# Kernel optimization log

Measured on AMD Instinct MI355X. Metric: run time of the kernel, lower is better.

Reference implementation:

```python
import jax, jax.numpy as jnp
import numpy as np

N_EMBED = 512  # codebook size per Quantize
EPS = 1e-8


def _quantize(x, embed):
    # x: (L, d) flattened tokens; embed: (d, K) codebook
    # squared euclidean distance via expansion (as in torch source)
    dist = (x * x).sum(1, keepdims=True) - 2.0 * (x @ embed) + (embed * embed).sum(0, keepdims=True)
    ind = jnp.argmin(dist, axis=1)                      # (L,)
    q = jnp.take(embed.T, ind, axis=0)                  # (L, d) embedding lookup
    diff = jnp.mean((jax.lax.stop_gradient(q) - x) ** 2)
    q_st = x + jax.lax.stop_gradient(q - x)             # straight-through
    return q_st, diff, ind


def _ot_score(x, embed):
    # x: (L, d); embed: (d, K). OT score = sum_k (1 - cos_sim) * softmax(x@embed / K)
    xn = x / (jnp.linalg.norm(x, axis=1, keepdims=True) + EPS)
    en = embed / (jnp.linalg.norm(embed, axis=0, keepdims=True) + EPS)
    cos_dissim = jax.lax.stop_gradient(1.0 - xn @ en)   # torch version uses .data (no grad)
    cnd = jax.nn.softmax((x @ embed) * (1.0 / embed.shape[1]), axis=1)
    return (cos_dissim * cnd).sum(1)                    # (L,)


def setup_inputs() -> dict:
    key = jax.random.key(0)
    k1, k2, k3, k4 = jax.random.split(key, 4)
    n_levels, B, L, d = 5, 128, 196, 64
    input_list = jax.random.normal(k1, (n_levels, B, L, d), dtype=jnp.float32)
    cb_top = jax.random.normal(k2, (15, d, N_EMBED), dtype=jnp.float32)        # quantize_list_5
    cb_lvl = jax.random.normal(k3, (4, 15, 2 * d, N_EMBED), dtype=jnp.float32)  # quantize_list_1..4
    label = jax.random.randint(k4, (B,), 0, 15, dtype=jnp.int32)
    return {"input_list": input_list, "cb_top": cb_top, "cb_lvl": cb_lvl, "label": label}


def reference(input_list, cb_top, cb_lvl, label):
    # Hierarchical switch-VQ encode (eval mode): top level quantized with per-class
    # codebook, then each lower level concatenated with top quantized code and
    # quantized with its own per-class codebook; last level also computes OT score.
    vq = jax.vmap(_quantize)
    emb_top = cb_top[label]                              # (B, 64, 512) per-sample codebook
    q4, d4, _ = vq(input_list[4], emb_top)               # (B, L, 64)
    diff = d4.sum()
    quants, ids = [], []
    ot_score = None
    for j in (3, 2, 1, 0):                               # quantize_list_4, _3, _2, _1
        x = jnp.concatenate([input_list[j], q4], axis=-1)  # (B, L, 128)
        emb = cb_lvl[j][label]                           # (B, 128, 512)
        q, d, i = vq(x, emb)
        diff = diff + d.sum()
        quants.append(q)
        ids.append(i)
        if j == 0:                                       # OT=True level
            ot_score = jax.vmap(_ot_score)(x, emb)       # (B, L)
    quant_list = jnp.stack(quants)                       # (4, B, L, 128)
    id_list = jnp.stack(ids)                             # (4, B, L)
    return quant_list, diff, id_list, ot_score
```

## Files before the change

kernel.cpp:

```cpp
#include <hip/hip_runtime.h>
#include <hip/hip_bf16.h>
#include <math.h>

#define B 128
#define L 196
#define K 512
#define NCLS 15
#define NT 32
#define NTILES 7

#define DIFF_OFF 12845056
#define ID_OFF   12845057
#define OT_OFF   12945409

#define WS_N2   0
#define WS_INVE 38400
#define WS_CBT  46080
#define CBT_LVL 491520
#define WS_EBT_BYTES ((size_t)(46080 + 4469760) * 4)
#define EBT_LVL_BYTES 983040

#define BAND 2.5f
#define CCAP 512

typedef __attribute__((ext_vector_type(8))) short s16x8;
typedef __attribute__((ext_vector_type(4))) float f32x4;
typedef __attribute__((ext_vector_type(4))) unsigned short u16x4;

__device__ inline unsigned short f2bf(float f) {
    __hip_bfloat16 h = __float2bfloat16(f);
    return *reinterpret_cast<unsigned short*>(&h);
}

__global__ __launch_bounds__(256) void precompute(
    const float* __restrict__ cb_top, const float* __restrict__ cb_lvl,
    float* __restrict__ ws)
{
    __shared__ float Ld[128][65];
    __shared__ float ps[64][4];
    const int m = blockIdx.x >> 3;
    const int c0 = (blockIdx.x & 7) * 64;
    const bool top = m < NCLS;
    const int D = top ? 64 : 128;
    const float* src = top ? cb_top + (size_t)m * 64 * K
                           : cb_lvl + (size_t)(m - NCLS) * 128 * K;
    float* cbT = ws + WS_CBT + (top ? (size_t)m * K * 64
                                    : (size_t)CBT_LVL + (size_t)(m - NCLS) * K * 128);
    unsigned short* ebt = (unsigned short*)((char*)ws + WS_EBT_BYTES +
        (top ? (size_t)m * K * 64 * 2
             : (size_t)EBT_LVL_BYTES + (size_t)(m - NCLS) * K * 128 * 2));
    const int tid = threadIdx.x;

    for (int e = tid; e < D * 64; e += 256) {
        int d = e >> 6, cc = e & 63;
        Ld[d][cc] = src[(size_t)d * K + c0 + cc];
    }
    __syncthreads();

    const int col = tid >> 2, q = tid & 3;
    const int seg = D >> 2;
    float ss = 0.f;
    for (int i = 0; i < seg; ++i) {
        int d = q * seg + i;
        float v = Ld[d][col];
        ss = fmaf(v, v, ss);
        cbT[(size_t)(c0 + col) * D + d] = v;
        ebt[(size_t)(c0 + col) * D + d] = f2bf(v);
    }
    ps[col][q] = ss;
    __syncthreads();
    if (tid < 64) {
        float n2 = (ps[tid][0] + ps[tid][1]) + (ps[tid][2] + ps[tid][3]);
        ws[WS_N2 + (size_t)m * K + c0 + tid] = n2;
        if (m >= NCLS && m < 2 * NCLS)
            ws[WS_INVE + (size_t)(m - NCLS) * K + c0 + tid] = 1.f / (sqrtf(n2) + 1e-8f);
    }
}

__global__ __launch_bounds__(256, 6) void vq_all(
    const float* __restrict__ input, const int* __restrict__ label,
    float* __restrict__ ws, float* __restrict__ out)
{
    __shared__ char uA[8192];
    __shared__ unsigned short xL_s[NT * 136];
    __shared__ float clv[CCAP];
    __shared__ unsigned int clist[CCAP];
    __shared__ float wmin_s[4][NT];
    __shared__ float rowMinG[NT];
    __shared__ unsigned long long best_s[NT];
    __shared__ float xn4_s[NT], xnL_s[NT], xnq_s[NT];
    __shared__ float otZ_s[NT], otW_s[NT];
    __shared__ float dacc_s;
    __shared__ int ccnt;

    unsigned short* x4_s = (unsigned short*)uA;
    float* q4f = (float*)uA;

    const int tid = threadIdx.x;
    const int t0 = blockIdx.x * NT;
    const int b = blockIdx.y;
    const int j = blockIdx.z;
    const bool OT = (j == 0);
    const bool addTop = (j == 3);
    const int c = label[b];

    const float* xin4 = input + ((size_t)(4 * B + b) * L) * 64;
    const float* xinj = input + ((size_t)(j * B + b) * L) * 64;
    const float* n2T = ws + WS_N2 + (size_t)c * K;
    const float* n2L = ws + WS_N2 + (size_t)(NCLS + j * NCLS + c) * K;
    const float* ive = ws + WS_INVE + (size_t)c * K;
    const float* cbT_T = ws + WS_CBT + (size_t)c * (K * 64);
    const float* cbT_L = ws + WS_CBT + CBT_LVL + (size_t)(j * NCLS + c) * (K * 128);
    const unsigned short* ebT =
        (const unsigned short*)((const char*)ws + WS_EBT_BYTES) + (size_t)c * (K * 64);
    const unsigned short* ebL =
        (const unsigned short*)((const char*)ws + WS_EBT_BYTES + EBT_LVL_BYTES) +
        (size_t)(j * NCLS + c) * (K * 128);

    const int wid = tid >> 6, lane = tid & 63, l15 = lane & 15, l4 = lane >> 4;

    if (tid < NT) {
        xn4_s[tid] = 0.f; xnL_s[tid] = 0.f; best_s[tid] = ~0ULL;
        otZ_s[tid] = 0.f; otW_s[tid] = 0.f;
    }
    if (tid == 0) { ccnt = 0; dacc_s = 0.f; }
    __syncthreads();

    for (int idx = tid; idx < NT * 16; idx += 256) {
        int row = idx >> 4, k4 = (idx & 15) << 2;
        int l = t0 + row;
        float4 v = make_float4(0.f, 0.f, 0.f, 0.f);
        if (l < L) {
            v = *(const float4*)(xin4 + (size_t)l * 64 + k4);
            atomicAdd(&xn4_s[row], v.x * v.x + v.y * v.y + v.z * v.z + v.w * v.w);
        }
        u16x4 h; h[0] = f2bf(v.x); h[1] = f2bf(v.y); h[2] = f2bf(v.z); h[3] = f2bf(v.w);
        *(u16x4*)&x4_s[row * 72 + k4] = h;
    }
    __syncthreads();

    float runMin[2][4];
    #pragma unroll
    for (int mi = 0; mi < 2; ++mi)
        #pragma unroll
        for (int r = 0; r < 4; ++r) runMin[mi][r] = 3.4e38f;

    for (int cc = 0; cc < 2; ++cc) {
        const int colbase = cc * 256 + wid * 64;
        float n2v[4];
        #pragma unroll
        for (int ni = 0; ni < 4; ++ni) n2v[ni] = n2T[colbase + ni * 16 + l15];
        f32x4 acc[2][4] = {};
        #pragma unroll
        for (int ks = 0; ks < 2; ++ks) {
            s16x8 av[2], bv[4];
            #pragma unroll
            for (int mi = 0; mi < 2; ++mi)
                av[mi] = *(const s16x8*)&x4_s[(mi * 16 + l15) * 72 + ks * 32 + l4 * 8];
            #pragma unroll
            for (int ni = 0; ni < 4; ++ni)
                bv[ni] = *(const s16x8*)&ebT[(size_t)(colbase + ni * 16 + l15) * 64 + ks * 32 + l4 * 8];
            #pragma unroll
            for (int mi = 0; mi < 2; ++mi)
                #pragma unroll
                for (int ni = 0; ni < 4; ++ni)
                    acc[mi][ni] = __builtin_amdgcn_mfma_f32_16x16x32_bf16(
                        av[mi], bv[ni], acc[mi][ni], 0, 0, 0);
        }
        #pragma unroll
        for (int mi = 0; mi < 2; ++mi) {
            #pragma unroll
            for (int r = 0; r < 4; ++r) {
                const int row = mi * 16 + l4 * 4 + r;
                float dv[4];
                #pragma unroll
                for (int ni = 0; ni < 4; ++ni)
                    dv[ni] = n2v[ni] - 2.f * acc[mi][ni][r];
                float mnW = fminf(fminf(dv[0], dv[1]), fminf(dv[2], dv[3]));
                #pragma unroll
                for (int s = 1; s <= 8; s <<= 1)
                    mnW = fminf(mnW, __shfl_xor(mnW, s, 64));
                runMin[mi][r] = fminf(runMin[mi][r], mnW);
                const float thr = runMin[mi][r] + BAND;
                if (t0 + row < L) {
                    #pragma unroll
                    for (int ni = 0; ni < 4; ++ni) {
                        if (dv[ni] <= thr) {
                            int pos = atomicAdd(&ccnt, 1);
                            if (pos < CCAP) {
                                clist[pos] = ((unsigned)row << 16) |
                                             (unsigned)(colbase + ni * 16 + l15);
                                clv[pos] = dv[ni];
                            }
                        }
                    }
                }
            }
        }
    }
    #pragma unroll
    for (int mi = 0; mi < 2; ++mi)
        #pragma unroll
        for (int r = 0; r < 4; ++r)
            if (l15 == 0) wmin_s[wid][mi * 16 + l4 * 4 + r] = runMin[mi][r];
    __syncthreads();
    if (tid < NT)
        rowMinG[tid] = fminf(fminf(wmin_s[0][tid], wmin_s[1][tid]),
                             fminf(wmin_s[2][tid], wmin_s[3][tid]));
    __syncthreads();

    {
        const int ncand = min(ccnt, CCAP);
        const int g = tid >> 4, li = tid & 15;
        for (int e = g; e < ncand; e += 16) {
            unsigned ent = clist[e];
            int row = ent >> 16, col = ent & 0xFFFF;
            if (clv[e] > rowMinG[row] + BAND) continue;
            int l = t0 + row;
            float4 xv = *(const float4*)(xin4 + (size_t)l * 64 + li * 4);
            float4 ev = *(const float4*)(cbT_T + (size_t)col * 64 + li * 4);
            float prod = xv.x * ev.x + xv.y * ev.y + xv.z * ev.z + xv.w * ev.w;
            #pragma unroll
            for (int s = 1; s <= 8; s <<= 1) prod += __shfl_xor(prod, s, 64);
            if (li == 0) {
                float dvE = n2T[col] - 2.f * prod;
                unsigned u = __float_as_uint(dvE);
                u = (u & 0x80000000u) ? ~u : (u | 0x80000000u);
                atomicMin(&best_s[row], ((unsigned long long)u << 32) | (unsigned)col);
            }
        }
    }
    __syncthreads();

    {
        const int g = tid >> 4, li = tid & 15;
        for (int rr = g; rr < NT; rr += 16) {
            int l = t0 + rr;
            unsigned long long key = best_s[rr];
            float4 ev = make_float4(0.f, 0.f, 0.f, 0.f);
            float dvE = 0.f;
            if (l < L) {
                unsigned col = (unsigned)(key & 0xFFFFFFFFull);
                unsigned u = (unsigned)(key >> 32);
                u = (u & 0x80000000u) ? (u & 0x7FFFFFFFu) : ~u;
                dvE = __uint_as_float(u);
                ev = *(const float4*)(cbT_T + (size_t)col * 64 + li * 4);
            }
            *(float4*)&q4f[rr * 64 + li * 4] = ev;
            u16x4 h; h[0] = f2bf(ev.x); h[1] = f2bf(ev.y); h[2] = f2bf(ev.z); h[3] = f2bf(ev.w);
            *(u16x4*)&xL_s[rr * 136 + 64 + li * 4] = h;
            float qs = ev.x * ev.x + ev.y * ev.y + ev.z * ev.z + ev.w * ev.w;
            #pragma unroll
            for (int s = 1; s <= 8; s <<= 1) qs += __shfl_xor(qs, s, 64);
            if (li == 0) {
                xnq_s[rr] = qs;
                if (addTop && l < L)
                    atomicAdd(&dacc_s, (dvE + xn4_s[rr]) * (1.f / (L * 64.f)));
            }
        }
    }
    __syncthreads();

    if (tid < NT) best_s[tid] = ~0ULL;
    if (tid == 0) ccnt = 0;
    for (int idx = tid; idx < NT * 16; idx += 256) {
        int row = idx >> 4, k4 = (idx & 15) << 2;
        int l = t0 + row;
        float4 v = make_float4(0.f, 0.f, 0.f, 0.f);
        if (l < L) {
            v = *(const float4*)(xinj + (size_t)l * 64 + k4);
            atomicAdd(&xnL_s[row], v.x * v.x + v.y * v.y + v.z * v.z + v.w * v.w);
        }
        u16x4 h; h[0] = f2bf(v.x); h[1] = f2bf(v.y); h[2] = f2bf(v.z); h[3] = f2bf(v.w);
        *(u16x4*)&xL_s[row * 136 + k4] = h;
    }
    __syncthreads();

    #pragma unroll
    for (int mi = 0; mi < 2; ++mi)
        #pragma unroll
        for (int r = 0; r < 4; ++r) runMin[mi][r] = 3.4e38f;

    for (int cc = 0; cc < 2; ++cc) {
        const int colbase = cc * 256 + wid * 64;
        float n2v[4], iv[4];
        #pragma unroll
        for (int ni = 0; ni < 4; ++ni) {
            n2v[ni] = n2L[colbase + ni * 16 + l15];
            if (OT) iv[ni] = ive[colbase + ni * 16 + l15];
        }
        f32x4 acc[2][4] = {};
        #pragma unroll
        for (int ks = 0; ks < 4; ++ks) {
            s16x8 av[2], bv[4];
            #pragma unroll
            for (int mi = 0; mi < 2; ++mi)
                av[mi] = *(const s16x8*)&xL_s[(mi * 16 + l15) * 136 + ks * 32 + l4 * 8];
            #pragma unroll
            for (int ni = 0; ni < 4; ++ni)
                bv[ni] = *(const s16x8*)&ebL[(size_t)(colbase + ni * 16 + l15) * 128 + ks * 32 + l4 * 8];
            #pragma unroll
            for (int mi = 0; mi < 2; ++mi)
                #pragma unroll
                for (int ni = 0; ni < 4; ++ni)
                    acc[mi][ni] = __builtin_amdgcn_mfma_f32_16x16x32_bf16(
                        av[mi], bv[ni], acc[mi][ni], 0, 0, 0);
        }
        #pragma unroll
        for (int mi = 0; mi < 2; ++mi) {
            #pragma unroll
            for (int r = 0; r < 4; ++r) {
                const int row = mi * 16 + l4 * 4 + r;
                float dv[4];
                #pragma unroll
                for (int ni = 0; ni < 4; ++ni)
                    dv[ni] = n2v[ni] - 2.f * acc[mi][ni][r];
                float mnW = fminf(fminf(dv[0], dv[1]), fminf(dv[2], dv[3]));
                #pragma unroll
                for (int s = 1; s <= 8; s <<= 1)
                    mnW = fminf(mnW, __shfl_xor(mnW, s, 64));
                runMin[mi][r] = fminf(runMin[mi][r], mnW);
                const float thr = runMin[mi][r] + BAND;
                if (t0 + row < L) {
                    #pragma unroll
                    for (int ni = 0; ni < 4; ++ni) {
                        if (dv[ni] <= thr) {
                            int pos = atomicAdd(&ccnt, 1);
                            if (pos < CCAP) {
                                clist[pos] = ((unsigned)row << 16) |
                                             (unsigned)(colbase + ni * 16 + l15);
                                clv[pos] = dv[ni];
                            }
                        }
                    }
                }
                if (OT) {
                    float xn = xnL_s[row] + xnq_s[row];
                    float ivx = 1.f / (sqrtf(xn) + 1e-8f);
                    float zloc = 0.f, wloc = 0.f;
                    #pragma unroll
                    for (int ni = 0; ni < 4; ++ni) {
                        float s = acc[mi][ni][r];
                        float e = __expf(s * (1.f / 512.f));
                        zloc += e;
                        wloc += (1.f - s * ivx * iv[ni]) * e;
                    }
                    #pragma unroll
                    for (int s = 1; s <= 8; s <<= 1) {
                        zloc += __shfl_xor(zloc, s, 64);
                        wloc += __shfl_xor(wloc, s, 64);
                    }
                    if (l15 == 0) {
                        atomicAdd(&otZ_s[row], zloc);
                        atomicAdd(&otW_s[row], wloc);
                    }
                }
            }
        }
    }
    #pragma unroll
    for (int mi = 0; mi < 2; ++mi)
        #pragma unroll
        for (int r = 0; r < 4; ++r)
            if (l15 == 0) wmin_s[wid][mi * 16 + l4 * 4 + r] = runMin[mi][r];
    __syncthreads();
    if (tid < NT)
        rowMinG[tid] = fminf(fminf(wmin_s[0][tid], wmin_s[1][tid]),
                             fminf(wmin_s[2][tid], wmin_s[3][tid]));
    __syncthreads();

    {
        const int ncand = min(ccnt, CCAP);
        const int g = tid >> 4, li = tid & 15;
        for (int e = g; e < ncand; e += 16) {
            unsigned ent = clist[e];
            int row = ent >> 16, col = ent & 0xFFFF;
            if (clv[e] > rowMinG[row] + BAND) continue;
            int l = t0 + row;
            int k = li * 8;
            float4 xa, xb;
            if (li < 8) {
                xa = *(const float4*)(xinj + (size_t)l * 64 + k);
                xb = *(const float4*)(xinj + (size_t)l * 64 + k + 4);
            } else {
                xa = *(const float4*)&q4f[row * 64 + (k - 64)];
                xb = *(const float4*)&q4f[row * 64 + (k - 60)];
            }
            float4 ea = *(const float4*)(cbT_L + (size_t)col * 128 + k);
            float4 eb = *(const float4*)(cbT_L + (size_t)col * 128 + k + 4);
            float prod = xa.x * ea.x + xa.y * ea.y + xa.z * ea.z + xa.w * ea.w +
                         xb.x * eb.x + xb.y * eb.y + xb.z * eb.z + xb.w * eb.w;
            #pragma unroll
            for (int s = 1; s <= 8; s <<= 1) prod += __shfl_xor(prod, s, 64);
            if (li == 0) {
                float dvE = n2L[col] - 2.f * prod;
                unsigned u = __float_as_uint(dvE);
                u = (u & 0x80000000u) ? ~u : (u | 0x80000000u);
                atomicMin(&best_s[row], ((unsigned long long)u << 32) | (unsigned)col);
            }
        }
    }
    __syncthreads();

    {
        const int slot = 3 - j;
        const int g = tid >> 4, li = tid & 15;
        for (int rr = g; rr < NT; rr += 16) {
            int l = t0 + rr;
            if (l >= L) continue;
            unsigned long long key = best_s[rr];
            unsigned col = (unsigned)(key & 0xFFFFFFFFull);
            unsigned u = (unsigned)(key >> 32);
            u = (u & 0x80000000u) ? (u & 0x7FFFFFFFu) : ~u;
            float dvE = __uint_as_float(u);
            float4 ea = *(const float4*)(cbT_L + (size_t)col * 128 + li * 8);
            float4 eb = *(const float4*)(cbT_L + (size_t)col * 128 + li * 8 + 4);
            float* dst = out + (((size_t)slot * B + b) * L + l) * 128 + li * 8;
            *(float4*)dst = ea;
            *(float4*)(dst + 4) = eb;
            if (li == 0) {
                out[ID_OFF + ((size_t)slot * B + b) * L + l] = (float)col;
                if (OT) out[OT_OFF + (size_t)b * L + l] = otW_s[rr] / otZ_s[rr];
                atomicAdd(&dacc_s, (dvE + xnL_s[rr] + xnq_s[rr]) * (1.f / (L * 128.f)));
            }
        }
    }
    __syncthreads();
    if (tid == 0) atomicAdd(out + DIFF_OFF, dacc_s);
}

extern "C" void kernel_launch(void* const* d_in, const int* in_sizes, int n_in,
                              void* d_out, int out_size, void* d_ws, size_t ws_size,
                              hipStream_t stream) {
    const float* input  = (const float*)d_in[0];
    const float* cb_top = (const float*)d_in[1];
    const float* cb_lvl = (const float*)d_in[2];
    const int*   label  = (const int*)d_in[3];
    float* out = (float*)d_out;
    float* ws  = (float*)d_ws;

    hipMemsetAsync(out + DIFF_OFF, 0, sizeof(float), stream);

    precompute<<<600, 256, 0, stream>>>(cb_top, cb_lvl, ws);
    vq_all<<<dim3(NTILES, B, 4), 256, 0, stream>>>(input, label, ws, out);
}
```

Measured before the change: 346.1 us.

## Group blocks by class label and stage inputs in shared memory for rescoring

A new small kernel sorts batch indices by label. vq_all then remaps block IDs, using an XCD-aware swizzle, so blocks sharing the same codebook run together and the codebook stays hot in L2. The fp32 input rows for level 4 and level j are also staged in shared memory, so candidate rescoring reads LDS instead of global memory, and the rescoring band is narrowed from 2.5 to 1.0 to cut candidate work. The trade-offs are one extra launch, more shared memory with occupancy lowered to 4 blocks per SIMD, and a narrower band that could miss the true argmin under bf16 error.

```diff
diff --git a/kernel.cpp b/kernel.cpp
--- a/kernel.cpp
+++ b/kernel.cpp
@@ -15,12 +15,14 @@
 
 #define WS_N2   0
 #define WS_INVE 38400
-#define WS_CBT  46080
+#define WS_PERM 46080
+#define WS_LAB  46208
+#define WS_CBT  46336
 #define CBT_LVL 491520
-#define WS_EBT_BYTES ((size_t)(46080 + 4469760) * 4)
+#define WS_EBT_BYTES ((size_t)(46336 + 4423680) * 4)
 #define EBT_LVL_BYTES 983040
 
-#define BAND 2.5f
+#define BAND 1.0f
 #define CCAP 512
 
 typedef __attribute__((ext_vector_type(8))) short s16x8;
@@ -30,6 +32,22 @@
 __device__ inline unsigned short f2bf(float f) {
     __hip_bfloat16 h = __float2bfloat16(f);
     return *reinterpret_cast<unsigned short*>(&h);
+}
+
+__global__ void sort_labels(const int* __restrict__ label, int* __restrict__ perm,
+                            int* __restrict__ lab) {
+    __shared__ int ls[B];
+    const int t = threadIdx.x;
+    ls[t] = label[t];
+    lab[t] = ls[t];
+    __syncthreads();
+    const int mine = ls[t];
+    int r = 0;
+    for (int i = 0; i < B; ++i) {
+        int li = ls[i];
+        r += (li < mine) || (li == mine && i < t);
+    }
+    perm[r] = t;
 }
 
 __global__ __launch_bounds__(256) void precompute(
@@ -77,11 +95,13 @@
     }
 }
 
-__global__ __launch_bounds__(256, 6) void vq_all(
-    const float* __restrict__ input, const int* __restrict__ label,
-    float* __restrict__ ws, float* __restrict__ out)
+__global__ __launch_bounds__(256, 4) void vq_all(
+    const float* __restrict__ input, float* __restrict__ ws,
+    float* __restrict__ out)
 {
-    __shared__ char uA[8192];
+    __shared__ float uA[NT][68];
+    __shared__ float xLf[NT][68];
+    __shared__ unsigned short x4_s[NT * 72];
     __shared__ unsigned short xL_s[NT * 136];
     __shared__ float clv[CCAP];
     __shared__ unsigned int clist[CCAP];
@@ -93,31 +113,33 @@
     __shared__ float dacc_s;
     __shared__ int ccnt;
 
-    unsigned short* x4_s = (unsigned short*)uA;
-    float* q4f = (float*)uA;
-
     const int tid = threadIdx.x;
-    const int t0 = blockIdx.x * NT;
-    const int b = blockIdx.y;
-    const int j = blockIdx.z;
+    const int hw = (int)blockIdx.x + 7 * (int)blockIdx.y + 896 * (int)blockIdx.z;
+    const int logical = (hw & 7) * 448 + (hw >> 3);
+    const int j = logical & 3;
+    const int rest = logical >> 2;
+    const int tile = rest % 7;
+    const int ys = rest / 7;
+    const int b = ((const int*)(ws + WS_PERM))[ys];
+    const int cls = ((const int*)(ws + WS_LAB))[b];
+
     const bool OT = (j == 0);
     const bool addTop = (j == 3);
-    const int c = label[b];
+    const int t0 = tile * NT;
+    const int wid = tid >> 6, lane = tid & 63, l15 = lane & 15, l4 = lane >> 4;
 
     const float* xin4 = input + ((size_t)(4 * B + b) * L) * 64;
     const float* xinj = input + ((size_t)(j * B + b) * L) * 64;
-    const float* n2T = ws + WS_N2 + (size_t)c * K;
-    const float* n2L = ws + WS_N2 + (size_t)(NCLS + j * NCLS + c) * K;
-    const float* ive = ws + WS_INVE + (size_t)c * K;
-    const float* cbT_T = ws + WS_CBT + (size_t)c * (K * 64);
-    const float* cbT_L = ws + WS_CBT + CBT_LVL + (size_t)(j * NCLS + c) * (K * 128);
+    const float* n2T = ws + WS_N2 + (size_t)cls * K;
+    const float* n2L = ws + WS_N2 + (size_t)(NCLS + j * NCLS + cls) * K;
+    const float* ive = ws + WS_INVE + (size_t)cls * K;
+    const float* cbT_T = ws + WS_CBT + (size_t)cls * (K * 64);
+    const float* cbT_L = ws + WS_CBT + CBT_LVL + (size_t)(j * NCLS + cls) * (K * 128);
     const unsigned short* ebT =
-        (const unsigned short*)((const char*)ws + WS_EBT_BYTES) + (size_t)c * (K * 64);
+        (const unsigned short*)((const char*)ws + WS_EBT_BYTES) + (size_t)cls * (K * 64);
     const unsigned short* ebL =
         (const unsigned short*)((const char*)ws + WS_EBT_BYTES + EBT_LVL_BYTES) +
-        (size_t)(j * NCLS + c) * (K * 128);
-
-    const int wid = tid >> 6, lane = tid & 63, l15 = lane & 15, l4 = lane >> 4;
+        (size_t)(j * NCLS + cls) * (K * 128);
 
     if (tid < NT) {
         xn4_s[tid] = 0.f; xnL_s[tid] = 0.f; best_s[tid] = ~0ULL;
@@ -134,8 +156,19 @@
             v = *(const float4*)(xin4 + (size_t)l * 64 + k4);
             atomicAdd(&xn4_s[row], v.x * v.x + v.y * v.y + v.z * v.z + v.w * v.w);
         }
+        *(float4*)&uA[row][k4] = v;
         u16x4 h; h[0] = f2bf(v.x); h[1] = f2bf(v.y); h[2] = f2bf(v.z); h[3] = f2bf(v.w);
         *(u16x4*)&x4_s[row * 72 + k4] = h;
+    }
+    for (int idx = tid; idx < NT * 16; idx += 256) {
+        int row = idx >> 4, k4 = (idx & 15) << 2;
+        int l = t0 + row;
+        float4 v = make_float4(0.f, 0.f, 0.f, 0.f);
+        if (l < L) {
+            v = *(const float4*)(xinj + (size_t)l * 64 + k4);
+            atomicAdd(&xnL_s[row], v.x * v.x + v.y * v.y + v.z * v.z + v.w * v.w);
+        }
+        *(float4*)&xLf[row][k4] = v;
     }
     __syncthreads();
 
@@ -216,8 +249,7 @@
             unsigned ent = clist[e];
             int row = ent >> 16, col = ent & 0xFFFF;
             if (clv[e] > rowMinG[row] + BAND) continue;
-            int l = t0 + row;
-            float4 xv = *(const float4*)(xin4 + (size_t)l * 64 + li * 4);
+            float4 xv = *(const float4*)&uA[row][li * 4];
             float4 ev = *(const float4*)(cbT_T + (size_t)col * 64 + li * 4);
             float prod = xv.x * ev.x + xv.y * ev.y + xv.z * ev.z + xv.w * ev.w;
             #pragma unroll
@@ -234,7 +266,9 @@
 
     {
         const int g = tid >> 4, li = tid & 15;
-        for (int rr = g; rr < NT; rr += 16) {
+        #pragma unroll
+        for (int rr0 = 0; rr0 < NT; rr0 += 16) {
+            const int rr = rr0 + g;
             int l = t0 + rr;
             unsigned long long key = best_s[rr];
             float4 ev = make_float4(0.f, 0.f, 0.f, 0.f);
@@ -246,12 +280,13 @@
                 dvE = __uint_as_float(u);
                 ev = *(const float4*)(cbT_T + (size_t)col * 64 + li * 4);
             }
-            *(float4*)&q4f[rr * 64 + li * 4] = ev;
+            float qs = ev.x * ev.x + ev.y * ev.y + ev.z * ev.z + ev.w * ev.w;
+            #pragma unroll
+            for (int s = 1; s <= 8; s <<= 1) qs += __shfl_xor(qs, s, 64);
+            __syncthreads();
+            *(float4*)&uA[rr][li * 4] = ev;
             u16x4 h; h[0] = f2bf(ev.x); h[1] = f2bf(ev.y); h[2] = f2bf(ev.z); h[3] = f2bf(ev.w);
             *(u16x4*)&xL_s[rr * 136 + 64 + li * 4] = h;
-            float qs = ev.x * ev.x + ev.y * ev.y + ev.z * ev.z + ev.w * ev.w;
-            #pragma unroll
-            for (int s = 1; s <= 8; s <<= 1) qs += __shfl_xor(qs, s, 64);
             if (li == 0) {
                 xnq_s[rr] = qs;
                 if (addTop && l < L)
@@ -265,12 +300,7 @@
     if (tid == 0) ccnt = 0;
     for (int idx = tid; idx < NT * 16; idx += 256) {
         int row = idx >> 4, k4 = (idx & 15) << 2;
-        int l = t0 + row;
-        float4 v = make_float4(0.f, 0.f, 0.f, 0.f);
-        if (l < L) {
-            v = *(const float4*)(xinj + (size_t)l * 64 + k4);
-            atomicAdd(&xnL_s[row], v.x * v.x + v.y * v.y + v.z * v.z + v.w * v.w);
-        }
+        float4 v = *(const float4*)&xLf[row][k4];
         u16x4 h; h[0] = f2bf(v.x); h[1] = f2bf(v.y); h[2] = f2bf(v.z); h[3] = f2bf(v.w);
         *(u16x4*)&xL_s[row * 136 + k4] = h;
     }
@@ -376,18 +406,10 @@
             unsigned ent = clist[e];
             int row = ent >> 16, col = ent & 0xFFFF;
             if (clv[e] > rowMinG[row] + BAND) continue;
-            int l = t0 + row;
-            int k = li * 8;
-            float4 xa, xb;
-            if (li < 8) {
-                xa = *(const float4*)(xinj + (size_t)l * 64 + k);
-                xb = *(const float4*)(xinj + (size_t)l * 64 + k + 4);
-            } else {
-                xa = *(const float4*)&q4f[row * 64 + (k - 64)];
-                xb = *(const float4*)&q4f[row * 64 + (k - 60)];
-            }
-            float4 ea = *(const float4*)(cbT_L + (size_t)col * 128 + k);
-            float4 eb = *(const float4*)(cbT_L + (size_t)col * 128 + k + 4);
+            float4 xa = *(const float4*)&xLf[row][li * 4];
+            float4 xb = *(const float4*)&uA[row][li * 4];
+            float4 ea = *(const float4*)(cbT_L + (size_t)col * 128 + li * 4);
+            float4 eb = *(const float4*)(cbT_L + (size_t)col * 128 + 64 + li * 4);
             float prod = xa.x * ea.x + xa.y * ea.y + xa.z * ea.z + xa.w * ea.w +
                          xb.x * eb.x + xb.y * eb.y + xb.z * eb.z + xb.w * eb.w;
             #pragma unroll
@@ -413,11 +435,11 @@
             unsigned u = (unsigned)(key >> 32);
             u = (u & 0x80000000u) ? (u & 0x7FFFFFFFu) : ~u;
             float dvE = __uint_as_float(u);
-            float4 ea = *(const float4*)(cbT_L + (size_t)col * 128 + li * 8);
-            float4 eb = *(const float4*)(cbT_L + (size_t)col * 128 + li * 8 + 4);
-            float* dst = out + (((size_t)slot * B + b) * L + l) * 128 + li * 8;
-            *(float4*)dst = ea;
-            *(float4*)(dst + 4) = eb;
+            float4 ea = *(const float4*)(cbT_L + (size_t)col * 128 + li * 4);
+            float4 eb = *(const float4*)(cbT_L + (size_t)col * 128 + 64 + li * 4);
+            float* dst = out + (((size_t)slot * B + b) * L + l) * 128;
+            *(float4*)(dst + li * 4) = ea;
+            *(float4*)(dst + 64 + li * 4) = eb;
             if (li == 0) {
                 out[ID_OFF + ((size_t)slot * B + b) * L + l] = (float)col;
                 if (OT) out[OT_OFF + (size_t)b * L + l] = otW_s[rr] / otZ_s[rr];
@@ -441,6 +463,7 @@
 
     hipMemsetAsync(out + DIFF_OFF, 0, sizeof(float), stream);
 
+    sort_labels<<<1, B, 0, stream>>>(label, (int*)(ws + WS_PERM), (int*)(ws + WS_LAB));
     precompute<<<600, 256, 0, stream>>>(cb_top, cb_lvl, ws);
-    vq_all<<<dim3(NTILES, B, 4), 256, 0, stream>>>(input, label, ws, out);
+    vq_all<<<dim3(NTILES, B, 4), 256, 0, stream>>>(input, ws, out);
 }
```

Measured after the change: 311.6 us. 1.11x faster.
